# Performance work log

Measured on AMD Instinct MI355X. Metric: run time of the kernel, lower is better.

Reference implementation:

```python
import jax, jax.numpy as jnp
import numpy as np

N_NODES = 100000
N_EDGES = 1600000
N_FEAT = 4
HIDDEN = 128
EMBED = 128
N_GRAPHS = 512


def setup_inputs() -> dict:
    key = jax.random.key(0)
    ks = jax.random.split(key, 12)
    x = jax.random.normal(ks[0], (N_NODES, N_FEAT), dtype=jnp.float32)
    edge_index = jax.random.randint(ks[1], (2, N_EDGES), 0, N_NODES, dtype=jnp.int64)
    batch = jnp.sort(jax.random.randint(ks[2], (N_NODES,), 0, N_GRAPHS, dtype=jnp.int64))
    def glorot(k, fan_in, fan_out):
        s = jnp.sqrt(6.0 / (fan_in + fan_out))
        return jax.random.uniform(k, (fan_in, fan_out), jnp.float32, -s, s)
    return {
        "x": x,
        "edge_index": edge_index,
        "batch": batch,
        "W_d1": glorot(ks[3], N_FEAT, N_FEAT),
        "b_d1": jnp.zeros((N_FEAT,), jnp.float32),
        "W_g1": glorot(ks[4], N_FEAT, HIDDEN),
        "b_g1": jnp.zeros((HIDDEN,), jnp.float32),
        "W_g2": glorot(ks[5], HIDDEN, HIDDEN),
        "b_g2": jnp.zeros((HIDDEN,), jnp.float32),
        "W_g3": glorot(ks[6], HIDDEN, HIDDEN),
        "b_g3": jnp.zeros((HIDDEN,), jnp.float32),
        "W_d2": glorot(ks[7], HIDDEN, EMBED),
        "b_d2": jnp.zeros((EMBED,), jnp.float32),
    }


def _gcn(x, W, b, src, dst, norm, n_nodes):
    # GCNConv: out[dst] += norm_e * (x @ W)[src], plus bias
    h = x @ W                      # [N, Dout]
    msg = h[src] * norm[:, None]   # [E+N, Dout] (self-loops included)
    out = jax.ops.segment_sum(msg, dst, num_segments=n_nodes)
    return out + b


def reference(x, edge_index, batch, W_d1, b_d1, W_g1, b_g1, W_g2, b_g2, W_g3, b_g3, W_d2, b_d2):
    n = x.shape[0]
    # add self-loops (PyG GCNConv default add_self_loops=True)
    loop = jnp.arange(n, dtype=edge_index.dtype)
    src = jnp.concatenate([edge_index[0], loop])
    dst = jnp.concatenate([edge_index[1], loop])
    # symmetric degree normalization: deg computed over target (col)
    deg = jax.ops.segment_sum(jnp.ones_like(dst, dtype=x.dtype), dst, num_segments=n)
    dis = jnp.where(deg > 0, jax.lax.rsqrt(jnp.maximum(deg, 1.0)), 0.0)
    norm = dis[src] * dis[dst]     # [E+N]

    h = jax.nn.relu(x @ W_d1 + b_d1)
    h = jax.nn.relu(_gcn(h, W_g1, b_g1, src, dst, norm, n))
    h = jax.nn.relu(_gcn(h, W_g2, b_g2, src, dst, norm, n))
    h = jax.nn.relu(_gcn(h, W_g3, b_g3, src, dst, norm, n))

    # global_mean_pool over batch assignment
    sums = jax.ops.segment_sum(h, batch, num_segments=N_GRAPHS)
    cnts = jax.ops.segment_sum(jnp.ones((n,), h.dtype), batch, num_segments=N_GRAPHS)
    pooled = sums / jnp.maximum(cnts, 1.0)[:, None]
    # dropout p=0.3 is identity in eval mode
    return pooled @ W_d2 + b_d2
```

## Files before the change

kernel.cpp:

```cpp
#include <hip/hip_runtime.h>
#include <hip/hip_fp16.h>


#define BSHIFT 8
#define BSZ    256
#define MAXBKT 512
#define CPAD   32
#define CAPSH  13

typedef _Float16 half8 __attribute__((ext_vector_type(8)));
typedef float f32x4 __attribute__((ext_vector_type(4)));

#define RFL __builtin_amdgcn_readfirstlane

__global__ __launch_bounds__(512) void k_prep(
        const float* __restrict__ x, const float* __restrict__ Wd1,
        const float* __restrict__ bd1, __half* __restrict__ h0,
        const float* __restrict__ W2, const float* __restrict__ W3,
        __half* __restrict__ WT2, __half* __restrict__ WT3,
        const int* __restrict__ batch, int* __restrict__ gs,
        const int* __restrict__ src, const int* __restrict__ dst,
        int* __restrict__ bktFill, int* __restrict__ staged,
        float* __restrict__ sums,
        int N, int NG, int E, int nbkt, int BINB, int L1B, int NB1) {
    __shared__ int hh[MAXBKT], base[MAXBKT], cur[MAXBKT];
    int bid = blockIdx.x;
    int t = threadIdx.x;
    if (bid < BINB) {
        for (int i = t; i < nbkt; i += 512) { hh[i] = 0; cur[i] = 0; }
        __syncthreads();
        int e0 = bid * 4096 + t;
#pragma unroll
        for (int k = 0; k < 8; k++) {
            int e = e0 + k * 512;
            if (e < E) atomicAdd(&hh[dst[e] >> BSHIFT], 1);
        }
        __syncthreads();
        for (int i = t; i < nbkt; i += 512)
            base[i] = hh[i] ? atomicAdd(&bktFill[(size_t)i * CPAD], hh[i]) : 0;
        __syncthreads();
#pragma unroll
        for (int k = 0; k < 8; k++) {
            int e = e0 + k * 512;
            if (e < E) {
                int d = dst[e], s = src[e];
                int b = d >> BSHIFT;
                int off = atomicAdd(&cur[b], 1);
                staged[((size_t)b << CAPSH) + base[b] + off] =
                    ((d & (BSZ - 1)) << 17) | s;
            }
        }
    } else if (bid < BINB + L1B) {
        int node = (bid - BINB) * 512 + t;
        if (node < N) {
            float4 xv = ((const float4*)x)[node];
            float h[4];
#pragma unroll
            for (int k = 0; k < 4; k++) {
                float v = xv.x * Wd1[k] + xv.y * Wd1[4 + k]
                        + xv.z * Wd1[8 + k] + xv.w * Wd1[12 + k] + bd1[k];
                h[k] = fmaxf(v, 0.f);
            }
            __half2 o01 = __floats2half2_rn(h[0], h[1]);
            __half2 o23 = __floats2half2_rn(h[2], h[3]);
            uint2 pk;
            pk.x = *(unsigned*)&o01; pk.y = *(unsigned*)&o23;
            *(uint2*)(h0 + (size_t)node * 4) = pk;
        }
    } else if (bid < BINB + L1B + 32) {
        int t2 = (bid - BINB - L1B) * 512 + t;
        int k = t2 >> 7, nn = t2 & 127;
        WT2[nn * 128 + k] = __float2half_rn(W2[t2]);
        WT3[nn * 128 + k] = __float2half_rn(W3[t2]);
    } else if (bid < BINB + L1B + 32 + NB1) {
        int i = (bid - BINB - L1B - 32) * 512 + t;
        if (i >= N) return;
        int b = batch[i];
        int prev = (i == 0) ? -1 : batch[i - 1];
        for (int g2 = prev + 1; g2 <= b; ++g2) gs[g2] = i;
        if (i == N - 1)
            for (int g2 = b + 1; g2 <= NG; ++g2) gs[g2] = N;
    } else {
        int idx = (bid - BINB - L1B - 32 - NB1) * 512 + t;
        if (idx < NG * 128) sums[idx] = 0.f;
    }
}

__global__ __launch_bounds__(1024) void k_fineB(
        const int* __restrict__ staged, const int* __restrict__ bktFill,
        int2* __restrict__ rpe, float* __restrict__ dis,
        int* __restrict__ col, const __half* __restrict__ h0,
        __half* __restrict__ h0s, int N) {
    __shared__ int sEnt[1 << CAPSH];
    __shared__ int cnt[BSZ];
    __shared__ int incl[BSZ];
    int b = blockIdx.x;
    int lo = b << CAPSH;
    int cntE = bktFill[(size_t)b * CPAD];
    int n0 = b << BSHIFT;
    int tid = threadIdx.x;
    if (tid < BSZ) cnt[tid] = 0;
    __syncthreads();
    for (int e = tid; e < cntE; e += 1024) {
        int v = staged[lo + e];
        sEnt[e] = v;
        atomicAdd(&cnt[v >> 17], 1);
    }
    __syncthreads();
    int v = 0;
    if (tid < BSZ) { v = cnt[tid]; incl[tid] = v; }
    for (int off = 1; off < BSZ; off <<= 1) {
        __syncthreads();
        int t = (tid < BSZ && tid >= off) ? incl[tid - off] : 0;
        __syncthreads();
        if (tid < BSZ) incl[tid] += t;
    }
    __syncthreads();
    int myofs = 0;
    if (tid < BSZ) {
        myofs = incl[tid] - v;
        int node = n0 + tid;
        if (node < N) {
            rpe[node] = make_int2(lo + myofs, lo + myofs + v);
            float dloc = rsqrtf((float)(v + 1));
            dis[node] = dloc;
            uint2 hv = *(const uint2*)(h0 + (size_t)node * 4);
            float2 a01 = __half22float2(*(__half2*)&hv.x);
            float2 a23 = __half22float2(*(__half2*)&hv.y);
            __half2 o01 = __floats2half2_rn(a01.x * dloc, a01.y * dloc);
            __half2 o23 = __floats2half2_rn(a23.x * dloc, a23.y * dloc);
            uint2 pk;
            pk.x = *(unsigned*)&o01; pk.y = *(unsigned*)&o23;
            *(uint2*)(h0s + (size_t)node * 4) = pk;
        }
    }
    __syncthreads();
    if (tid < BSZ) { incl[tid] = myofs; cnt[tid] = 0; }
    __syncthreads();
    for (int e = tid; e < cntE; e += 1024) {
        int ent = sEnt[e];
        int dl = ent >> 17;
        int pos = lo + incl[dl] + atomicAdd(&cnt[dl], 1);
        col[pos] = ent & 0x1FFFF;
    }
}

__device__ __forceinline__ void addv4(float a[4], uint2 v) {
    float2 x01 = __half22float2(*(__half2*)&v.x);
    float2 x23 = __half22float2(*(__half2*)&v.y);
    a[0] += x01.x; a[1] += x01.y; a[2] += x23.x; a[3] += x23.y;
}

__global__ __launch_bounds__(256) void k_agg4(
        const __half* __restrict__ h0s, const int2* __restrict__ rpe,
        const float* __restrict__ dis, const int* __restrict__ col,
        float4* __restrict__ agg4, int N) {
    int n = blockIdx.x * 256 + threadIdx.x;
    if (n >= N) return;
    int2 re = rpe[n];
    float di = dis[n];
    float a[4];
    {
        uint2 sv = *(const uint2*)(h0s + (size_t)n * 4);
        float2 s01 = __half22float2(*(__half2*)&sv.x);
        float2 s23 = __half22float2(*(__half2*)&sv.y);
        a[0] = s01.x; a[1] = s01.y; a[2] = s23.x; a[3] = s23.y;
    }
    int e = re.x, r1 = re.y;
    for (; e + 3 < r1; e += 4) {
        int c0 = col[e], c1 = col[e + 1], c2 = col[e + 2], c3 = col[e + 3];
        uint2 v0 = *(const uint2*)(h0s + (size_t)c0 * 4);
        uint2 v1 = *(const uint2*)(h0s + (size_t)c1 * 4);
        uint2 v2 = *(const uint2*)(h0s + (size_t)c2 * 4);
        uint2 v3 = *(const uint2*)(h0s + (size_t)c3 * 4);
        addv4(a, v0); addv4(a, v1); addv4(a, v2); addv4(a, v3);
    }
    for (; e < r1; ++e) {
        uint2 v0 = *(const uint2*)(h0s + (size_t)col[e] * 4);
        addv4(a, v0);
    }
    agg4[n] = make_float4(di * a[0], di * a[1], di * a[2], di * a[3]);
}

__global__ __launch_bounds__(256) void k_mmL1(
        const float4* __restrict__ agg4, const float* __restrict__ Wg1,
        const float* __restrict__ b1, const __half* __restrict__ WT2,
        const float* __restrict__ dis, __half* __restrict__ gout, int n) {
    __shared__ float sW[512];
    __shared__ float sB[128];
    __shared__ _Float16 sH[16 * 136];
    __shared__ _Float16 sO[16 * 136];
    __shared__ float sDis[16];
    int t = threadIdx.x;
    sW[t] = Wg1[t];
    sW[t + 256] = Wg1[t + 256];
    if (t < 128) sB[t] = b1[t];
    int node0 = blockIdx.x * 16;
    int row = t >> 4, seg = t & 15;
    if (t < 16) sDis[t] = (node0 + t < n) ? dis[node0 + t] : 0.f;
    int nodeR = node0 + row;
    float4 av = (nodeR < n) ? agg4[nodeR] : make_float4(0.f, 0.f, 0.f, 0.f);
    __syncthreads();
    half8 hv;
#pragma unroll
    for (int u = 0; u < 8; u++) {
        int j = seg * 8 + u;
        float vv = sB[j] + av.x * sW[j] + av.y * sW[128 + j]
                 + av.z * sW[256 + j] + av.w * sW[384 + j];
        hv[u] = (_Float16)fmaxf(vv, 0.f);
    }
    *(half8*)&sH[row * 136 + seg * 8] = hv;
    __syncthreads();
    int wave = t >> 6, lane = t & 63;
    int q = lane >> 4, c = lane & 15;
    int n0 = wave * 32;
    f32x4 acc0 = {0.f, 0.f, 0.f, 0.f}, acc1 = {0.f, 0.f, 0.f, 0.f};
#pragma unroll
    for (int ks = 0; ks < 4; ks++) {
        int k0 = ks * 32;
        half8 a  = *(half8*)&sH[c * 136 + k0 + q * 8];
        half8 b0 = *(const half8*)(WT2 + (size_t)(n0 + c) * 128 + k0 + q * 8);
        half8 b1v = *(const half8*)(WT2 + (size_t)(n0 + 16 + c) * 128 + k0 + q * 8);
        acc0 = __builtin_amdgcn_mfma_f32_16x16x32_f16(a, b0, acc0, 0, 0, 0);
        acc1 = __builtin_amdgcn_mfma_f32_16x16x32_f16(a, b1v, acc1, 0, 0, 0);
    }
#pragma unroll
    for (int r = 0; r < 4; r++) {
        int rr = q * 4 + r;
        sO[rr * 136 + n0 + c]      = (_Float16)(acc0[r] * sDis[rr]);
        sO[rr * 136 + n0 + 16 + c] = (_Float16)(acc1[r] * sDis[rr]);
    }
    __syncthreads();
    if (nodeR < n)
        *(uint4*)(gout + (size_t)nodeR * 128 + seg * 8) =
            *(uint4*)&sO[row * 136 + seg * 8];
}

__device__ __forceinline__ void acc4r(float acc[4], uint2 v) {
    float2 a01 = __half22float2(*(__half2*)&v.x);
    float2 a23 = __half22float2(*(__half2*)&v.y);
    acc[0] += a01.x; acc[1] += a01.y; acc[2] += a23.x; acc[3] += a23.y;
}

__device__ __forceinline__ void agg_node4(
        const __half* __restrict__ g, const int* __restrict__ col,
        int r0, int r1, int node, int hf, int sl, float acc[4]) {
    uint2 mr = *(const uint2*)(g + (size_t)node * 128 + sl * 4);
    float2 m01 = __half22float2(*(__half2*)&mr.x);
    float2 m23 = __half22float2(*(__half2*)&mr.y);
    float sw = hf ? 0.f : 1.f;
    acc[0] = sw * m01.x; acc[1] = sw * m01.y;
    acc[2] = sw * m23.x; acc[3] = sw * m23.y;
    int e = r0;
    for (; e + 7 < r1; e += 8) {
        int sa0 = RFL(col[e]),     sb0 = RFL(col[e + 1]);
        int sa1 = RFL(col[e + 2]), sb1 = RFL(col[e + 3]);
        int sa2 = RFL(col[e + 4]), sb2 = RFL(col[e + 5]);
        int sa3 = RFL(col[e + 6]), sb3 = RFL(col[e + 7]);
        int s0 = hf ? sb0 : sa0;
        int s1 = hf ? sb1 : sa1;
        int s2 = hf ? sb2 : sa2;
        int s3 = hf ? sb3 : sa3;
        uint2 r0v = *(const uint2*)(g + (size_t)s0 * 128 + sl * 4);
        uint2 r1v = *(const uint2*)(g + (size_t)s1 * 128 + sl * 4);
        uint2 r2v = *(const uint2*)(g + (size_t)s2 * 128 + sl * 4);
        uint2 r3v = *(const uint2*)(g + (size_t)s3 * 128 + sl * 4);
        acc4r(acc, r0v); acc4r(acc, r1v); acc4r(acc, r2v); acc4r(acc, r3v);
    }
    for (; e + 1 < r1; e += 2) {
        int sa = RFL(col[e]), sb = RFL(col[e + 1]);
        int s = hf ? sb : sa;
        uint2 rv = *(const uint2*)(g + (size_t)s * 128 + sl * 4);
        acc4r(acc, rv);
    }
    if (e < r1) {
        int sa = RFL(col[e]);
        uint2 rv = *(const uint2*)(g + (size_t)sa * 128 + sl * 4);
        if (!hf) acc4r(acc, rv);
    }
#pragma unroll
    for (int k = 0; k < 4; k++) acc[k] += __shfl_xor(acc[k], 32);
}

__global__ __launch_bounds__(256) void k_aggmm(
        const __half* __restrict__ gin, const int2* __restrict__ rpe,
        const int* __restrict__ col, const float* __restrict__ dis,
        const float* __restrict__ bias, const __half* __restrict__ WT,
        __half* __restrict__ gout, int n) {
    __shared__ _Float16 sH[16 * 136];
    __shared__ _Float16 sO[16 * 136];
    __shared__ float sDis[16];
    int t = threadIdx.x;
    int wave = t >> 6, lane = t & 63;
    int hf = lane >> 5, sl = lane & 31;
    int node0 = blockIdx.x * 16;
    if (t < 16) sDis[t] = (node0 + t < n) ? dis[node0 + t] : 0.f;
    float4 bb = ((const float4*)bias)[sl];
#pragma unroll
    for (int i = 0; i < 4; i++) {
        int node = RFL(node0 + wave * 4 + i);
        if (node < n) {
            int2 re = rpe[node];
            int r0 = RFL(re.x);
            int r1 = RFL(re.y);
            float di = dis[node];
            float acc[4];
            agg_node4(gin, col, r0, r1, node, hf, sl, acc);
            if (hf == 0) {
                int lr = wave * 4 + i;
                __half2 o01 = __floats2half2_rn(
                    fmaxf(fmaf(di, acc[0], bb.x), 0.f),
                    fmaxf(fmaf(di, acc[1], bb.y), 0.f));
                __half2 o23 = __floats2half2_rn(
                    fmaxf(fmaf(di, acc[2], bb.z), 0.f),
                    fmaxf(fmaf(di, acc[3], bb.w), 0.f));
                uint2 pk;
                pk.x = *(unsigned*)&o01; pk.y = *(unsigned*)&o23;
                *(uint2*)&sH[lr * 136 + sl * 4] = pk;
            }
        }
    }
    __syncthreads();
    int q = lane >> 4, c = lane & 15;
    int n0 = wave * 32;
    f32x4 acc0 = {0.f, 0.f, 0.f, 0.f}, acc1 = {0.f, 0.f, 0.f, 0.f};
#pragma unroll
    for (int ks = 0; ks < 4; ks++) {
        int k0 = ks * 32;
        half8 a  = *(half8*)&sH[c * 136 + k0 + q * 8];
        half8 b0 = *(const half8*)(WT + (size_t)(n0 + c) * 128 + k0 + q * 8);
        half8 b1 = *(const half8*)(WT + (size_t)(n0 + 16 + c) * 128 + k0 + q * 8);
        acc0 = __builtin_amdgcn_mfma_f32_16x16x32_f16(a, b0, acc0, 0, 0, 0);
        acc1 = __builtin_amdgcn_mfma_f32_16x16x32_f16(a, b1, acc1, 0, 0, 0);
    }
#pragma unroll
    for (int r = 0; r < 4; r++) {
        int rr = q * 4 + r;
        sO[rr * 136 + n0 + c]      = (_Float16)(acc0[r] * sDis[rr]);
        sO[rr * 136 + n0 + 16 + c] = (_Float16)(acc1[r] * sDis[rr]);
    }
    __syncthreads();
    int lr2 = t >> 4, seg = t & 15;
    int rowN = node0 + lr2;
    if (rowN < n)
        *(uint4*)(gout + (size_t)rowN * 128 + seg * 8) =
            *(uint4*)&sO[lr2 * 136 + seg * 8];
}

__global__ __launch_bounds__(256) void k_aggsum(
        const __half* __restrict__ gin, const int2* __restrict__ rpe,
        const int* __restrict__ col, const float* __restrict__ dis,
        const float* __restrict__ bias, const int* __restrict__ batch,
        float* __restrict__ sums, int n) {
    __shared__ float ls[4][128];
    int t = threadIdx.x;
    int wave = t >> 6, lane = t & 63;
    int hf = lane >> 5, sl = lane & 31;
    int nodeBase = blockIdx.x * 16;
    if (nodeBase >= n) return;
    int lastNode = min(nodeBase + 15, n - 1);
    int b0 = RFL(batch[nodeBase]);
    bool uni = (RFL(batch[lastNode]) == b0);
    float4 bb = ((const float4*)bias)[sl];
    float sx[4] = {0.f, 0.f, 0.f, 0.f};
    int curb = b0;
#pragma unroll
    for (int i = 0; i < 4; i++) {
        int node = RFL(nodeBase + wave * 4 + i);
        if (node < n) {
            int2 re = rpe[node];
            int r0 = RFL(re.x);
            int r1 = RFL(re.y);
            float di = dis[node];
            float acc[4];
            agg_node4(gin, col, r0, r1, node, hf, sl, acc);
            float o0 = fmaxf(fmaf(di, acc[0], bb.x), 0.f);
            float o1 = fmaxf(fmaf(di, acc[1], bb.y), 0.f);
            float o2 = fmaxf(fmaf(di, acc[2], bb.z), 0.f);
            float o3 = fmaxf(fmaf(di, acc[3], bb.w), 0.f);
            if (!uni) {
                int b = RFL(batch[node]);
                if (b != curb) {
                    if (hf == 0) {
                        atomicAdd(&sums[(size_t)curb * 128 + sl * 4 + 0], sx[0]);
                        atomicAdd(&sums[(size_t)curb * 128 + sl * 4 + 1], sx[1]);
                        atomicAdd(&sums[(size_t)curb * 128 + sl * 4 + 2], sx[2]);
                        atomicAdd(&sums[(size_t)curb * 128 + sl * 4 + 3], sx[3]);
                    }
                    sx[0] = sx[1] = sx[2] = sx[3] = 0.f;
                    curb = b;
                }
            }
            sx[0] += o0; sx[1] += o1; sx[2] += o2; sx[3] += o3;
        }
    }
    if (uni) {
        if (hf == 0) {
            ls[wave][sl * 4 + 0] = sx[0];
            ls[wave][sl * 4 + 1] = sx[1];
            ls[wave][sl * 4 + 2] = sx[2];
            ls[wave][sl * 4 + 3] = sx[3];
        }
        __syncthreads();
        if (t < 128) {
            float v = ls[0][t] + ls[1][t] + ls[2][t] + ls[3][t];
            atomicAdd(&sums[(size_t)b0 * 128 + t], v);
        }
    } else {
        if (hf == 0) {
            atomicAdd(&sums[(size_t)curb * 128 + sl * 4 + 0], sx[0]);
            atomicAdd(&sums[(size_t)curb * 128 + sl * 4 + 1], sx[1]);
            atomicAdd(&sums[(size_t)curb * 128 + sl * 4 + 2], sx[2]);
            atomicAdd(&sums[(size_t)curb * 128 + sl * 4 + 3], sx[3]);
        }
    }
}

__global__ __launch_bounds__(128) void k_head(
        const float* __restrict__ sums, const int* __restrict__ gs,
        const float* __restrict__ Wd2, const float* __restrict__ bd2,
        float* __restrict__ out) {
    int gidx = blockIdx.x;
    int j = threadIdx.x;
    int c = gs[gidx + 1] - gs[gidx];
    float inv = 1.0f / (float)(c > 1 ? c : 1);
    __shared__ float sp[128];
    sp[j] = sums[(size_t)gidx * 128 + j] * inv;
    __syncthreads();
    float o = bd2[j];
#pragma unroll 8
    for (int k = 0; k < 128; k++) o = fmaf(sp[k], Wd2[k * 128 + j], o);
    out[gidx * 128 + j] = o;
}

extern "C" void kernel_launch(void* const* d_in, const int* in_sizes, int n_in,
                              void* d_out, int out_size, void* d_ws, size_t ws_size,
                              hipStream_t stream) {
    const float* x   = (const float*)d_in[0];
    const int*  ei   = (const int*)d_in[1];
    const int* batch = (const int*)d_in[2];
    const float* Wd1 = (const float*)d_in[3];
    const float* bd1 = (const float*)d_in[4];
    const float* Wg1 = (const float*)d_in[5];
    const float* bg1 = (const float*)d_in[6];
    const float* Wg2 = (const float*)d_in[7];
    const float* bg2 = (const float*)d_in[8];
    const float* Wg3 = (const float*)d_in[9];
    const float* bg3 = (const float*)d_in[10];
    const float* Wd2 = (const float*)d_in[11];
    const float* bd2 = (const float*)d_in[12];
    float* out = (float*)d_out;

    int N  = in_sizes[0] / 4;
    int E  = in_sizes[1] / 2;
    int NG = out_size / 128;
    const int* srcIdx = ei;
    const int* dstIdx = ei + E;
    int nbkt = (N + BSZ - 1) >> BSHIFT;

    char* p = (char*)d_ws;
    auto alloc = [&](size_t bytes) -> char* {
        char* r = p;
        p += (bytes + 255) & ~(size_t)255;
        return r;
    };
    int*    bktFill = (int*)alloc((size_t)nbkt * CPAD * 4);
    int*    staged  = (int*)alloc(((size_t)nbkt << CAPSH) * 4);
    int*    col     = (int*)alloc(((size_t)nbkt << CAPSH) * 4);
    int2*   rpe     = (int2*)alloc((size_t)N * 8);
    float*  dis     = (float*)alloc((size_t)N * 4);
    int*    gs      = (int*)alloc(((size_t)NG + 1) * 4);
    float*  sums    = (float*)alloc((size_t)NG * 128 * 4);
    __half* WT2     = (__half*)alloc(16384 * 2);
    __half* WT3     = (__half*)alloc(16384 * 2);
    __half* gA      = (__half*)alloc((size_t)N * 128 * 2);
    __half* gB      = (__half*)alloc((size_t)N * 128 * 2);
    __half* h0      = (__half*)alloc((size_t)N * 4 * 2);
    __half* h0s     = (__half*)alloc((size_t)N * 4 * 2);
    float4* agg4    = (float4*)alloc((size_t)N * 16);
    (void)ws_size; (void)n_in;

    int BINB = (E + 4095) / 4096;
    int L1B  = (N + 511) / 512;
    int NB1  = (N + 511) / 512;
    int ZB   = (NG * 128 + 511) / 512;
    int prepB = BINB + L1B + 32 + NB1 + ZB;
    int nb16 = (N + 15) / 16;

    hipMemsetAsync(bktFill, 0, (size_t)nbkt * CPAD * 4, stream);

    k_prep<<<prepB, 512, 0, stream>>>(x, Wd1, bd1, h0, Wg2, Wg3, WT2, WT3,
                                      batch, gs, srcIdx, dstIdx, bktFill,
                                      staged, sums, N, NG, E, nbkt,
                                      BINB, L1B, NB1);
    k_fineB<<<nbkt, 1024, 0, stream>>>(staged, bktFill, rpe, dis, col,
                                       h0, h0s, N);

    k_agg4<<<(N + 255) / 256, 256, 0, stream>>>(h0s, rpe, dis, col, agg4, N);
    k_mmL1<<<nb16, 256, 0, stream>>>(agg4, Wg1, bg1, WT2, dis, gB, N);
    k_aggmm<<<nb16, 256, 0, stream>>>(gB, rpe, col, dis, bg2, WT3, gA, N);
    k_aggsum<<<nb16, 256, 0, stream>>>(gA, rpe, col, dis, bg3, batch, sums, N);

    k_head<<<NG, 128, 0, stream>>>(sums, gs, Wd2, bd2, out);
}
```

Measured before the change: 307.5 us.

## Fuse layer-1 aggregation into matmul kernel and stage CSR column scatter in LDS

The per-node 4-feature aggregation kernel is merged into the layer-1 matmul kernel. Each wave now aggregates 4 nodes with lanes spread over edges and a shuffle reduction, which removes the agg4 intermediate buffer and one kernel launch. In k_fineB, column indices are scattered into shared memory and then written out contiguously, so global writes are coalesced instead of random. The trade-offs are that only 4 feature lanes are used per wave reduction, and that low-degree nodes leave most lanes idle during aggregation.

```diff
diff --git a/kernel.cpp b/kernel.cpp
--- a/kernel.cpp
+++ b/kernel.cpp
@@ -91,7 +91,7 @@
         int2* __restrict__ rpe, float* __restrict__ dis,
         int* __restrict__ col, const __half* __restrict__ h0,
         __half* __restrict__ h0s, int N) {
-    __shared__ int sEnt[1 << CAPSH];
+    __shared__ int sCol[1 << CAPSH];
     __shared__ int cnt[BSZ];
     __shared__ int incl[BSZ];
     int b = blockIdx.x;
@@ -101,11 +101,8 @@
     int tid = threadIdx.x;
     if (tid < BSZ) cnt[tid] = 0;
     __syncthreads();
-    for (int e = tid; e < cntE; e += 1024) {
-        int v = staged[lo + e];
-        sEnt[e] = v;
-        atomicAdd(&cnt[v >> 17], 1);
-    }
+    for (int e = tid; e < cntE; e += 1024)
+        atomicAdd(&cnt[staged[lo + e] >> 17], 1);
     __syncthreads();
     int v = 0;
     if (tid < BSZ) { v = cnt[tid]; incl[tid] = v; }
@@ -138,11 +135,14 @@
     if (tid < BSZ) { incl[tid] = myofs; cnt[tid] = 0; }
     __syncthreads();
     for (int e = tid; e < cntE; e += 1024) {
-        int ent = sEnt[e];
+        int ent = staged[lo + e];
         int dl = ent >> 17;
-        int pos = lo + incl[dl] + atomicAdd(&cnt[dl], 1);
-        col[pos] = ent & 0x1FFFF;
-    }
+        int pos = incl[dl] + atomicAdd(&cnt[dl], 1);
+        sCol[pos] = ent & 0x1FFFF;
+    }
+    __syncthreads();
+    for (int e = tid; e < cntE; e += 1024)
+        col[lo + e] = sCol[e];
 }
 
 __device__ __forceinline__ void addv4(float a[4], uint2 v) {
@@ -151,84 +151,92 @@
     a[0] += x01.x; a[1] += x01.y; a[2] += x23.x; a[3] += x23.y;
 }
 
-__global__ __launch_bounds__(256) void k_agg4(
+__global__ __launch_bounds__(256) void k_aggL1(
         const __half* __restrict__ h0s, const int2* __restrict__ rpe,
         const float* __restrict__ dis, const int* __restrict__ col,
-        float4* __restrict__ agg4, int N) {
-    int n = blockIdx.x * 256 + threadIdx.x;
-    if (n >= N) return;
-    int2 re = rpe[n];
-    float di = dis[n];
-    float a[4];
-    {
-        uint2 sv = *(const uint2*)(h0s + (size_t)n * 4);
-        float2 s01 = __half22float2(*(__half2*)&sv.x);
-        float2 s23 = __half22float2(*(__half2*)&sv.y);
-        a[0] = s01.x; a[1] = s01.y; a[2] = s23.x; a[3] = s23.y;
-    }
-    int e = re.x, r1 = re.y;
-    for (; e + 3 < r1; e += 4) {
-        int c0 = col[e], c1 = col[e + 1], c2 = col[e + 2], c3 = col[e + 3];
-        uint2 v0 = *(const uint2*)(h0s + (size_t)c0 * 4);
-        uint2 v1 = *(const uint2*)(h0s + (size_t)c1 * 4);
-        uint2 v2 = *(const uint2*)(h0s + (size_t)c2 * 4);
-        uint2 v3 = *(const uint2*)(h0s + (size_t)c3 * 4);
-        addv4(a, v0); addv4(a, v1); addv4(a, v2); addv4(a, v3);
-    }
-    for (; e < r1; ++e) {
-        uint2 v0 = *(const uint2*)(h0s + (size_t)col[e] * 4);
-        addv4(a, v0);
-    }
-    agg4[n] = make_float4(di * a[0], di * a[1], di * a[2], di * a[3]);
-}
-
-__global__ __launch_bounds__(256) void k_mmL1(
-        const float4* __restrict__ agg4, const float* __restrict__ Wg1,
-        const float* __restrict__ b1, const __half* __restrict__ WT2,
-        const float* __restrict__ dis, __half* __restrict__ gout, int n) {
+        const float* __restrict__ Wg1, const float* __restrict__ b1,
+        const __half* __restrict__ WT2, __half* __restrict__ gout, int n) {
     __shared__ float sW[512];
     __shared__ float sB[128];
+    __shared__ float sAgg[16][4];
+    __shared__ float sDis[16];
     __shared__ _Float16 sH[16 * 136];
     __shared__ _Float16 sO[16 * 136];
-    __shared__ float sDis[16];
     int t = threadIdx.x;
     sW[t] = Wg1[t];
     sW[t + 256] = Wg1[t + 256];
     if (t < 128) sB[t] = b1[t];
     int node0 = blockIdx.x * 16;
+    if (t < 16) sDis[t] = (node0 + t < n) ? dis[node0 + t] : 0.f;
+    if (t < 64) sAgg[t >> 2][t & 3] = 0.f;
+    __syncthreads();
+    int wave = t >> 6, lane = t & 63;
+#pragma unroll
+    for (int i = 0; i < 4; i++) {
+        int nl = wave * 4 + i;
+        int node = RFL(node0 + nl);
+        if (node < n) {
+            int2 re = rpe[node];
+            int r0 = RFL(re.x), r1 = RFL(re.y);
+            float a[4] = {0.f, 0.f, 0.f, 0.f};
+            for (int base = r0; base < r1; base += 64) {
+                int e = base + lane;
+                if (e < r1) {
+                    uint2 vv = *(const uint2*)(h0s + (size_t)col[e] * 4);
+                    addv4(a, vv);
+                }
+            }
+#pragma unroll
+            for (int k = 0; k < 4; k++) {
+                a[k] += __shfl_xor(a[k], 1);
+                a[k] += __shfl_xor(a[k], 2);
+                a[k] += __shfl_xor(a[k], 4);
+                a[k] += __shfl_xor(a[k], 8);
+                a[k] += __shfl_xor(a[k], 16);
+                a[k] += __shfl_xor(a[k], 32);
+            }
+            uint2 sv = *(const uint2*)(h0s + (size_t)node * 4);
+            float2 s01 = __half22float2(*(__half2*)&sv.x);
+            float2 s23 = __half22float2(*(__half2*)&sv.y);
+            a[0] += s01.x; a[1] += s01.y; a[2] += s23.x; a[3] += s23.y;
+            float di = dis[node];
+            float av = (lane == 0) ? a[0] : (lane == 1) ? a[1]
+                     : (lane == 2) ? a[2] : a[3];
+            if (lane < 4) sAgg[nl][lane] = av * di;
+        }
+    }
+    __syncthreads();
     int row = t >> 4, seg = t & 15;
-    if (t < 16) sDis[t] = (node0 + t < n) ? dis[node0 + t] : 0.f;
     int nodeR = node0 + row;
-    float4 av = (nodeR < n) ? agg4[nodeR] : make_float4(0.f, 0.f, 0.f, 0.f);
-    __syncthreads();
+    float4 av4 = make_float4(sAgg[row][0], sAgg[row][1],
+                             sAgg[row][2], sAgg[row][3]);
     half8 hv;
 #pragma unroll
     for (int u = 0; u < 8; u++) {
         int j = seg * 8 + u;
-        float vv = sB[j] + av.x * sW[j] + av.y * sW[128 + j]
-                 + av.z * sW[256 + j] + av.w * sW[384 + j];
+        float vv = sB[j] + av4.x * sW[j] + av4.y * sW[128 + j]
+                 + av4.z * sW[256 + j] + av4.w * sW[384 + j];
         hv[u] = (_Float16)fmaxf(vv, 0.f);
     }
     *(half8*)&sH[row * 136 + seg * 8] = hv;
     __syncthreads();
-    int wave = t >> 6, lane = t & 63;
     int q = lane >> 4, c = lane & 15;
-    int n0 = wave * 32;
+    int n0c = wave * 32;
     f32x4 acc0 = {0.f, 0.f, 0.f, 0.f}, acc1 = {0.f, 0.f, 0.f, 0.f};
 #pragma unroll
     for (int ks = 0; ks < 4; ks++) {
         int k0 = ks * 32;
         half8 a  = *(half8*)&sH[c * 136 + k0 + q * 8];
-        half8 b0 = *(const half8*)(WT2 + (size_t)(n0 + c) * 128 + k0 + q * 8);
-        half8 b1v = *(const half8*)(WT2 + (size_t)(n0 + 16 + c) * 128 + k0 + q * 8);
+        half8 b0 = *(const half8*)(WT2 + (size_t)(n0c + c) * 128 + k0 + q * 8);
+        half8 b1v = *(const half8*)(WT2 + (size_t)(n0c + 16 + c) * 128 + k0 + q * 8);
         acc0 = __builtin_amdgcn_mfma_f32_16x16x32_f16(a, b0, acc0, 0, 0, 0);
         acc1 = __builtin_amdgcn_mfma_f32_16x16x32_f16(a, b1v, acc1, 0, 0, 0);
     }
 #pragma unroll
     for (int r = 0; r < 4; r++) {
         int rr = q * 4 + r;
-        sO[rr * 136 + n0 + c]      = (_Float16)(acc0[r] * sDis[rr]);
-        sO[rr * 136 + n0 + 16 + c] = (_Float16)(acc1[r] * sDis[rr]);
+        sO[rr * 136 + n0c + c]      = (_Float16)(acc0[r] * sDis[rr]);
+        sO[rr * 136 + n0c + 16 + c] = (_Float16)(acc1[r] * sDis[rr]);
     }
     __syncthreads();
     if (nodeR < n)
@@ -477,7 +485,6 @@
     __half* gB      = (__half*)alloc((size_t)N * 128 * 2);
     __half* h0      = (__half*)alloc((size_t)N * 4 * 2);
     __half* h0s     = (__half*)alloc((size_t)N * 4 * 2);
-    float4* agg4    = (float4*)alloc((size_t)N * 16);
     (void)ws_size; (void)n_in;
 
     int BINB = (E + 4095) / 4096;
@@ -496,8 +503,8 @@
     k_fineB<<<nbkt, 1024, 0, stream>>>(staged, bktFill, rpe, dis, col,
                                        h0, h0s, N);
 
-    k_agg4<<<(N + 255) / 256, 256, 0, stream>>>(h0s, rpe, dis, col, agg4, N);
-    k_mmL1<<<nb16, 256, 0, stream>>>(agg4, Wg1, bg1, WT2, dis, gB, N);
+    k_aggL1<<<nb16, 256, 0, stream>>>(h0s, rpe, dis, col, Wg1, bg1, WT2,
+                                      gB, N);
     k_aggmm<<<nb16, 256, 0, stream>>>(gB, rpe, col, dis, bg2, WT3, gA, N);
     k_aggsum<<<nb16, 256, 0, stream>>>(gA, rpe, col, dis, bg3, batch, sums, N);
 
```

Measured after the change: 315.7 us. +2.7%, slower.

## Quantize intermediate node features to int8 with per-node scales for gathers

Applied to the files above, without the earlier changes.

The 128-wide intermediate features written by the matmul kernels are stored as int8 with one float scale per node, replacing fp16. The aggregation gathers then read 4 bytes per lane instead of 8 and dequantize with an fma against the per-node scale. This halves the bytes moved by the bandwidth-bound edge gathers, at the cost of an extra scale load per edge and lower numerical precision in the hidden activations.

```diff
diff --git a/kernel.cpp b/kernel.cpp
--- a/kernel.cpp
+++ b/kernel.cpp
@@ -185,7 +185,8 @@
 __global__ __launch_bounds__(256) void k_mmL1(
         const float4* __restrict__ agg4, const float* __restrict__ Wg1,
         const float* __restrict__ b1, const __half* __restrict__ WT2,
-        const float* __restrict__ dis, __half* __restrict__ gout, int n) {
+        const float* __restrict__ dis, signed char* __restrict__ qout,
+        float* __restrict__ scOut, int n) {
     __shared__ float sW[512];
     __shared__ float sB[128];
     __shared__ _Float16 sH[16 * 136];
@@ -231,26 +232,49 @@
         sO[rr * 136 + n0 + 16 + c] = (_Float16)(acc1[r] * sDis[rr]);
     }
     __syncthreads();
-    if (nodeR < n)
-        *(uint4*)(gout + (size_t)nodeR * 128 + seg * 8) =
-            *(uint4*)&sO[row * 136 + seg * 8];
-}
-
-__device__ __forceinline__ void acc4r(float acc[4], uint2 v) {
-    float2 a01 = __half22float2(*(__half2*)&v.x);
-    float2 a23 = __half22float2(*(__half2*)&v.y);
-    acc[0] += a01.x; acc[1] += a01.y; acc[2] += a23.x; acc[3] += a23.y;
-}
-
-__device__ __forceinline__ void agg_node4(
-        const __half* __restrict__ g, const int* __restrict__ col,
+    half8 ov = *(half8*)&sO[row * 136 + seg * 8];
+    float vv[8];
+    float lmax = 0.f;
+#pragma unroll
+    for (int u = 0; u < 8; u++) {
+        vv[u] = (float)ov[u];
+        lmax = fmaxf(lmax, fabsf(vv[u]));
+    }
+#pragma unroll
+    for (int m = 1; m < 16; m <<= 1)
+        lmax = fmaxf(lmax, __shfl_xor(lmax, m));
+    float inv = lmax > 0.f ? 127.f / lmax : 0.f;
+    unsigned d0 = 0, d1 = 0;
+#pragma unroll
+    for (int u = 0; u < 4; u++) {
+        int q0 = __float2int_rn(vv[u] * inv);
+        int q1 = __float2int_rn(vv[u + 4] * inv);
+        d0 |= ((unsigned)(q0 & 0xff)) << (8 * u);
+        d1 |= ((unsigned)(q1 & 0xff)) << (8 * u);
+    }
+    if (nodeR < n) {
+        *(uint2*)(qout + (size_t)nodeR * 128 + seg * 8) = make_uint2(d0, d1);
+        if (seg == 0) scOut[nodeR] = lmax * (1.f / 127.f);
+    }
+}
+
+__device__ __forceinline__ void accq(float acc[4], unsigned u, float w) {
+    acc[0] = fmaf(w, (float)(int)(signed char)(u), acc[0]);
+    acc[1] = fmaf(w, (float)(int)(signed char)(u >> 8), acc[1]);
+    acc[2] = fmaf(w, (float)(int)(signed char)(u >> 16), acc[2]);
+    acc[3] = fmaf(w, (float)(int)(signed char)(u >> 24), acc[3]);
+}
+
+__device__ __forceinline__ void agg_node4q(
+        const signed char* __restrict__ g, const float* __restrict__ sc,
+        const int* __restrict__ col,
         int r0, int r1, int node, int hf, int sl, float acc[4]) {
-    uint2 mr = *(const uint2*)(g + (size_t)node * 128 + sl * 4);
-    float2 m01 = __half22float2(*(__half2*)&mr.x);
-    float2 m23 = __half22float2(*(__half2*)&mr.y);
-    float sw = hf ? 0.f : 1.f;
-    acc[0] = sw * m01.x; acc[1] = sw * m01.y;
-    acc[2] = sw * m23.x; acc[3] = sw * m23.y;
+    acc[0] = acc[1] = acc[2] = acc[3] = 0.f;
+    {
+        unsigned su = *(const unsigned*)(g + (size_t)node * 128 + sl * 4);
+        float wself = hf ? 0.f : sc[node];
+        accq(acc, su, wself);
+    }
     int e = r0;
     for (; e + 7 < r1; e += 8) {
         int sa0 = RFL(col[e]),     sb0 = RFL(col[e + 1]);
@@ -261,32 +285,37 @@
         int s1 = hf ? sb1 : sa1;
         int s2 = hf ? sb2 : sa2;
         int s3 = hf ? sb3 : sa3;
-        uint2 r0v = *(const uint2*)(g + (size_t)s0 * 128 + sl * 4);
-        uint2 r1v = *(const uint2*)(g + (size_t)s1 * 128 + sl * 4);
-        uint2 r2v = *(const uint2*)(g + (size_t)s2 * 128 + sl * 4);
-        uint2 r3v = *(const uint2*)(g + (size_t)s3 * 128 + sl * 4);
-        acc4r(acc, r0v); acc4r(acc, r1v); acc4r(acc, r2v); acc4r(acc, r3v);
+        float w0 = sc[s0], w1 = sc[s1], w2 = sc[s2], w3 = sc[s3];
+        unsigned u0 = *(const unsigned*)(g + (size_t)s0 * 128 + sl * 4);
+        unsigned u1 = *(const unsigned*)(g + (size_t)s1 * 128 + sl * 4);
+        unsigned u2 = *(const unsigned*)(g + (size_t)s2 * 128 + sl * 4);
+        unsigned u3 = *(const unsigned*)(g + (size_t)s3 * 128 + sl * 4);
+        accq(acc, u0, w0); accq(acc, u1, w1);
+        accq(acc, u2, w2); accq(acc, u3, w3);
     }
     for (; e + 1 < r1; e += 2) {
         int sa = RFL(col[e]), sb = RFL(col[e + 1]);
         int s = hf ? sb : sa;
-        uint2 rv = *(const uint2*)(g + (size_t)s * 128 + sl * 4);
-        acc4r(acc, rv);
+        float w = sc[s];
+        unsigned u = *(const unsigned*)(g + (size_t)s * 128 + sl * 4);
+        accq(acc, u, w);
     }
     if (e < r1) {
         int sa = RFL(col[e]);
-        uint2 rv = *(const uint2*)(g + (size_t)sa * 128 + sl * 4);
-        if (!hf) acc4r(acc, rv);
+        float w = hf ? 0.f : sc[sa];
+        unsigned u = *(const unsigned*)(g + (size_t)sa * 128 + sl * 4);
+        accq(acc, u, w);
     }
 #pragma unroll
     for (int k = 0; k < 4; k++) acc[k] += __shfl_xor(acc[k], 32);
 }
 
 __global__ __launch_bounds__(256) void k_aggmm(
-        const __half* __restrict__ gin, const int2* __restrict__ rpe,
-        const int* __restrict__ col, const float* __restrict__ dis,
-        const float* __restrict__ bias, const __half* __restrict__ WT,
-        __half* __restrict__ gout, int n) {
+        const signed char* __restrict__ qin, const float* __restrict__ scIn,
+        const int2* __restrict__ rpe, const int* __restrict__ col,
+        const float* __restrict__ dis, const float* __restrict__ bias,
+        const __half* __restrict__ WT, signed char* __restrict__ qout,
+        float* __restrict__ scOut, int n) {
     __shared__ _Float16 sH[16 * 136];
     __shared__ _Float16 sO[16 * 136];
     __shared__ float sDis[16];
@@ -305,7 +334,7 @@
             int r1 = RFL(re.y);
             float di = dis[node];
             float acc[4];
-            agg_node4(gin, col, r0, r1, node, hf, sl, acc);
+            agg_node4q(qin, scIn, col, r0, r1, node, hf, sl, acc);
             if (hf == 0) {
                 int lr = wave * 4 + i;
                 __half2 o01 = __floats2half2_rn(
@@ -342,16 +371,37 @@
     __syncthreads();
     int lr2 = t >> 4, seg = t & 15;
     int rowN = node0 + lr2;
-    if (rowN < n)
-        *(uint4*)(gout + (size_t)rowN * 128 + seg * 8) =
-            *(uint4*)&sO[lr2 * 136 + seg * 8];
+    half8 ov = *(half8*)&sO[lr2 * 136 + seg * 8];
+    float vv[8];
+    float lmax = 0.f;
+#pragma unroll
+    for (int u = 0; u < 8; u++) {
+        vv[u] = (float)ov[u];
+        lmax = fmaxf(lmax, fabsf(vv[u]));
+    }
+#pragma unroll
+    for (int m = 1; m < 16; m <<= 1)
+        lmax = fmaxf(lmax, __shfl_xor(lmax, m));
+    float inv = lmax > 0.f ? 127.f / lmax : 0.f;
+    unsigned d0 = 0, d1 = 0;
+#pragma unroll
+    for (int u = 0; u < 4; u++) {
+        int q0 = __float2int_rn(vv[u] * inv);
+        int q1 = __float2int_rn(vv[u + 4] * inv);
+        d0 |= ((unsigned)(q0 & 0xff)) << (8 * u);
+        d1 |= ((unsigned)(q1 & 0xff)) << (8 * u);
+    }
+    if (rowN < n) {
+        *(uint2*)(qout + (size_t)rowN * 128 + seg * 8) = make_uint2(d0, d1);
+        if (seg == 0) scOut[rowN] = lmax * (1.f / 127.f);
+    }
 }
 
 __global__ __launch_bounds__(256) void k_aggsum(
-        const __half* __restrict__ gin, const int2* __restrict__ rpe,
-        const int* __restrict__ col, const float* __restrict__ dis,
-        const float* __restrict__ bias, const int* __restrict__ batch,
-        float* __restrict__ sums, int n) {
+        const signed char* __restrict__ qin, const float* __restrict__ scIn,
+        const int2* __restrict__ rpe, const int* __restrict__ col,
+        const float* __restrict__ dis, const float* __restrict__ bias,
+        const int* __restrict__ batch, float* __restrict__ sums, int n) {
     __shared__ float ls[4][128];
     int t = threadIdx.x;
     int wave = t >> 6, lane = t & 63;
@@ -373,7 +423,7 @@
             int r1 = RFL(re.y);
             float di = dis[node];
             float acc[4];
-            agg_node4(gin, col, r0, r1, node, hf, sl, acc);
+            agg_node4q(qin, scIn, col, r0, r1, node, hf, sl, acc);
             float o0 = fmaxf(fmaf(di, acc[0], bb.x), 0.f);
             float o1 = fmaxf(fmaf(di, acc[1], bb.y), 0.f);
             float o2 = fmaxf(fmaf(di, acc[2], bb.z), 0.f);
@@ -473,8 +523,10 @@
     float*  sums    = (float*)alloc((size_t)NG * 128 * 4);
     __half* WT2     = (__half*)alloc(16384 * 2);
     __half* WT3     = (__half*)alloc(16384 * 2);
-    __half* gA      = (__half*)alloc((size_t)N * 128 * 2);
-    __half* gB      = (__half*)alloc((size_t)N * 128 * 2);
+    signed char* qB = (signed char*)alloc((size_t)N * 128);
+    signed char* qA = (signed char*)alloc((size_t)N * 128);
+    float*  scB     = (float*)alloc((size_t)N * 4);
+    float*  scA     = (float*)alloc((size_t)N * 4);
     __half* h0      = (__half*)alloc((size_t)N * 4 * 2);
     __half* h0s     = (__half*)alloc((size_t)N * 4 * 2);
     float4* agg4    = (float4*)alloc((size_t)N * 16);
@@ -497,9 +549,11 @@
                                        h0, h0s, N);
 
     k_agg4<<<(N + 255) / 256, 256, 0, stream>>>(h0s, rpe, dis, col, agg4, N);
-    k_mmL1<<<nb16, 256, 0, stream>>>(agg4, Wg1, bg1, WT2, dis, gB, N);
-    k_aggmm<<<nb16, 256, 0, stream>>>(gB, rpe, col, dis, bg2, WT3, gA, N);
-    k_aggsum<<<nb16, 256, 0, stream>>>(gA, rpe, col, dis, bg3, batch, sums, N);
+    k_mmL1<<<nb16, 256, 0, stream>>>(agg4, Wg1, bg1, WT2, dis, qB, scB, N);
+    k_aggmm<<<nb16, 256, 0, stream>>>(qB, scB, rpe, col, dis, bg2, WT3,
+                                      qA, scA, N);
+    k_aggsum<<<nb16, 256, 0, stream>>>(qA, scA, rpe, col, dis, bg3, batch,
+                                       sums, N);
 
     k_head<<<NG, 128, 0, stream>>>(sums, gs, Wd2, bd2, out);
 }
```

New measurement: 282.5 us. 1.09x faster.
